# Optimization experiments

Measured on AMD Instinct MI355X. Metric: run time of the kernel, lower is better.

Reference implementation:

```python
import jax, jax.numpy as jnp
import numpy as np

B, L, D, H, F, NL = 8, 1024, 640, 10, 1280, 6
DH = D // H
WINDOW = 64  # spatial-neighbor band half-width
NEG = -1e9


def layer_norm(x, g, b, eps=1e-5):
    m = jnp.mean(x, axis=-1, keepdims=True)
    v = jnp.mean((x - m) ** 2, axis=-1, keepdims=True)
    return (x - m) * jax.lax.rsqrt(v + eps) * g + b


def setup_inputs() -> dict:
    key = jax.random.key(0)
    ks = jax.random.split(key, 20)
    s = 0.02
    x = jax.random.normal(ks[0], (B, L, D), jnp.float32)
    y = jax.random.normal(ks[1], (B, L, D), jnp.float32)
    idx = jnp.arange(L)
    band = jnp.abs(idx[:, None] - idx[None, :]) > WINDOW  # True = disallowed
    x_attn_mask = jnp.broadcast_to(band, (B, L, L))
    y_attn_mask = jnp.broadcast_to(band, (B, L, L))
    x_pad_mask = jnp.zeros((B, L), bool)
    y_pad_mask = jnp.zeros((B, L), bool)
    # stacked per-layer encoder params (torch Linear convention: out = x @ W.T + b)
    params = dict(
        Wqkv=jax.random.normal(ks[2], (NL, 3 * D, D), jnp.float32) * s,
        bqkv=jnp.zeros((NL, 3 * D), jnp.float32),
        Wo=jax.random.normal(ks[3], (NL, D, D), jnp.float32) * s,
        bo=jnp.zeros((NL, D), jnp.float32),
        ln1_g=jnp.ones((NL, D), jnp.float32),
        ln1_b=jnp.zeros((NL, D), jnp.float32),
        W1=jax.random.normal(ks[4], (NL, F, D), jnp.float32) * s,
        b1=jnp.zeros((NL, F), jnp.float32),
        W2=jax.random.normal(ks[5], (NL, D, F), jnp.float32) * s,
        b2=jnp.zeros((NL, D), jnp.float32),
        ln2_g=jnp.ones((NL, D), jnp.float32),
        ln2_b=jnp.zeros((NL, D), jnp.float32),
        lne_g=jnp.ones((D,), jnp.float32),
        lne_b=jnp.zeros((D,), jnp.float32),
        We=jax.random.normal(ks[6], (D, D), jnp.float32) * s,
        be=jnp.zeros((D,), jnp.float32),
    )
    return dict(x=x, x_pad_mask=x_pad_mask, x_attn_mask=x_attn_mask,
                y=y, y_pad_mask=y_pad_mask, y_attn_mask=y_attn_mask, **params)


def _encoder(h, mask_bias, Wqkv, bqkv, Wo, bo, ln1_g, ln1_b, W1, b1, W2, b2, ln2_g, ln2_b):
    scale = 1.0 / np.sqrt(DH)

    def step(h, p):
        (wqkv, bq, wo, bo_, g1, be1, w1, bb1, w2, bb2, g2, be2) = p
        qkv = jnp.einsum('bld,ed->ble', h, wqkv) + bq
        q, k, v = jnp.split(qkv, 3, axis=-1)
        q = q.reshape(B, L, H, DH)
        k = k.reshape(B, L, H, DH)
        v = v.reshape(B, L, H, DH)
        scores = jnp.einsum('blhd,bmhd->bhlm', q, k) * scale + mask_bias  # (B,H,L,L)
        attn = jax.nn.softmax(scores, axis=-1)
        o = jnp.einsum('bhlm,bmhd->blhd', attn, v).reshape(B, L, D)
        o = jnp.einsum('bld,ed->ble', o, wo) + bo_
        h = layer_norm(h + o, g1, be1)  # post-LN (torch default norm_first=False)
        ff = jax.nn.relu(jnp.einsum('bld,fd->blf', h, w1) + bb1)
        ff = jnp.einsum('blf,df->bld', ff, w2) + bb2
        h = layer_norm(h + ff, g2, be2)
        return h, None

    ps = (Wqkv, bqkv, Wo, bo, ln1_g, ln1_b, W1, b1, W2, b2, ln2_g, ln2_b)
    h, _ = jax.lax.scan(step, h, ps)
    return h


def _embed_pool(x, pad_mask, attn_mask, P):
    # bool mask semantics (torch): True = not allowed to attend
    blocked = attn_mask | pad_mask[:, None, :]            # (B,L,L)
    mask_bias = jnp.where(blocked, NEG, 0.0)[:, None]      # (B,1,L,L), shared by heads
    h = _encoder(x, mask_bias, P['Wqkv'], P['bqkv'], P['Wo'], P['bo'],
                 P['ln1_g'], P['ln1_b'], P['W1'], P['b1'], P['W2'], P['b2'],
                 P['ln2_g'], P['ln2_b'])
    pooled = h.sum(axis=1)                                 # (B,D)
    e = layer_norm(pooled, P['lne_g'], P['lne_b'])
    return jax.nn.relu(e @ P['We'].T + P['be'])


def reference(x, x_pad_mask, x_attn_mask, y, y_pad_mask, y_attn_mask,
              Wqkv, bqkv, Wo, bo, ln1_g, ln1_b, W1, b1, W2, b2, ln2_g, ln2_b,
              lne_g, lne_b, We, be):
    P = dict(Wqkv=Wqkv, bqkv=bqkv, Wo=Wo, bo=bo, ln1_g=ln1_g, ln1_b=ln1_b,
             W1=W1, b1=b1, W2=W2, b2=b2, ln2_g=ln2_g, ln2_b=ln2_b,
             lne_g=lne_g, lne_b=lne_b, We=We, be=be)
    ex = _embed_pool(x, x_pad_mask, x_attn_mask, P)
    ey = _embed_pool(y, y_pad_mask, y_attn_mask, P)
    eps = 1e-8
    nx = jnp.maximum(jnp.linalg.norm(ex, axis=-1), eps)
    ny = jnp.maximum(jnp.linalg.norm(ey, axis=-1), eps)
    return jnp.sum(ex * ey, axis=-1) / (nx * ny)  # (B,)
```

## Files before the change

kernel.cpp:

```cpp
#include <hip/hip_runtime.h>


#define LSEQ   1024
#define DMODEL 640
#define NHEAD  10
#define DHEAD  64
#define NLAYER 6
#define BDIM   8
#define FDIM   1280
#define MROWS  (BDIM * LSEQ)

typedef __attribute__((ext_vector_type(8))) _Float16 half8;
typedef __attribute__((ext_vector_type(4))) float    floatx4;

__device__ __forceinline__ void async_copy16(const void* g, void* l) {
  __builtin_amdgcn_global_load_lds(
      (const __attribute__((address_space(1))) void*)g,
      (__attribute__((address_space(3))) void*)l, 16, 0, 0);
}

template <bool RELU, bool RESADD, bool SPLITK>
__global__ __launch_bounds__(256) void gemm_bt(const _Float16* __restrict__ A,
                                               const _Float16* __restrict__ Bw,
                                               const float* __restrict__ bias,
                                               const _Float16* __restrict__ res,
                                               _Float16* __restrict__ Cout,
                                               int M, int N, int K, int ld) {
  __shared__ _Float16 As[2][128 * 32];
  __shared__ _Float16 Bs[2][128 * 32];
  const int m0 = blockIdx.x * 128, n0 = blockIdx.y * 128;
  const int kz = SPLITK ? blockIdx.z : 0;
  const int tid = threadIdx.x;
  const int w = tid >> 6, lane = tid & 63;
  const int quad = lane >> 4, l16 = lane & 15;
  const int wm = w >> 1, wn = w & 1;

  floatx4 acc[4][4];
#pragma unroll
  for (int i = 0; i < 4; i++)
#pragma unroll
    for (int j = 0; j < 4; j++) acc[i][j] = (floatx4){0.f, 0.f, 0.f, 0.f};

  const int arow = w * 16 + (lane >> 2);
  const int kswz = ((lane & 3) ^ ((lane >> 3) & 3)) * 8;
  const _Float16* ag = A + (size_t)(m0 + arow) * ld + kz * K + kswz;
  const _Float16* bg = Bw + (size_t)(n0 + arow) * ld + kz * K + kswz;
  const size_t krows = (size_t)64 * ld;
  const int lofs0 = (w * 16) * 32;
  const int lofs1 = (64 + w * 16) * 32;

  const int fro = l16 * 32 + ((quad ^ ((l16 >> 1) & 3)) * 8);

  const int nIter = K >> 5;
  async_copy16(ag, &As[0][lofs0]);
  async_copy16(ag + krows, &As[0][lofs1]);
  async_copy16(bg, &Bs[0][lofs0]);
  async_copy16(bg + krows, &Bs[0][lofs1]);
  ag += 32; bg += 32;

  for (int i = 0; i < nIter; i++) {
    __syncthreads();
    if (i + 1 < nIter) {
      const int nb = (i + 1) & 1;
      async_copy16(ag, &As[nb][lofs0]);
      async_copy16(ag + krows, &As[nb][lofs1]);
      async_copy16(bg, &Bs[nb][lofs0]);
      async_copy16(bg + krows, &Bs[nb][lofs1]);
      ag += 32; bg += 32;
    }
    const _Float16* as = As[i & 1];
    const _Float16* bs = Bs[i & 1];
    half8 af[4], bf[4];
#pragma unroll
    for (int mt = 0; mt < 4; mt++)
      af[mt] = *(const half8*)&as[(wm * 64 + mt * 16) * 32 + fro];
#pragma unroll
    for (int nt = 0; nt < 4; nt++)
      bf[nt] = *(const half8*)&bs[(wn * 64 + nt * 16) * 32 + fro];
#pragma unroll
    for (int mt = 0; mt < 4; mt++)
#pragma unroll
      for (int nt = 0; nt < 4; nt++)
        acc[mt][nt] = __builtin_amdgcn_mfma_f32_16x16x32_f16(af[mt], bf[nt], acc[mt][nt], 0, 0, 0);
  }

  const bool lead = (!SPLITK) || (kz == 0);
  _Float16* outp = Cout + (SPLITK ? (size_t)kz * ((size_t)M * N) : 0);
  float bv[4];
#pragma unroll
  for (int nt = 0; nt < 4; nt++)
    bv[nt] = lead ? bias[n0 + wn * 64 + nt * 16 + l16] : 0.f;
#pragma unroll
  for (int mt = 0; mt < 4; mt++) {
#pragma unroll
    for (int reg = 0; reg < 4; reg++) {
      const int row = m0 + wm * 64 + mt * 16 + quad * 4 + reg;
#pragma unroll
      for (int nt = 0; nt < 4; nt++) {
        const int col = n0 + wn * 64 + nt * 16 + l16;
        float v = acc[mt][nt][reg] + bv[nt];
        if (RESADD) { if (lead) v += (float)res[(size_t)row * N + col]; }
        if (RELU) v = fmaxf(v, 0.f);
        outp[(size_t)row * N + col] = (_Float16)v;
      }
    }
  }
}

__global__ __launch_bounds__(256) void attn_kernel(const _Float16* __restrict__ qkv,
                                                   _Float16* __restrict__ o) {
  __shared__ _Float16 Qs[64 * 72];
  __shared__ _Float16 KP[192 * 72];
  __shared__ _Float16 Vt[64 * 200];
  const int qb = blockIdx.x, h = blockIdx.y, b = blockIdx.z;
  const int q0 = qb * 64;
  const int kc0 = (q0 - 64 > 0) ? q0 - 64 : 0;
  const int kend = (q0 + 128 < LSEQ) ? q0 + 128 : LSEQ;
  const int cnt = kend - kc0;
  const int tid = threadIdx.x;

  for (int c = tid; c < 512; c += 256) {
    const int row = c >> 3, ch = c & 7;
    *(uint4*)&Qs[row * 72 + ch * 8] =
        *(const uint4*)(qkv + (size_t)(b * LSEQ + q0 + row) * (3 * DMODEL) + h * DHEAD + ch * 8);
  }
  for (int c = tid; c < 1536; c += 256) {
    const int row = c >> 3, ch = c & 7;
    uint4 v = {0u, 0u, 0u, 0u};
    if (row < cnt)
      v = *(const uint4*)(qkv + (size_t)(b * LSEQ + kc0 + row) * (3 * DMODEL) + DMODEL + h * DHEAD + ch * 8);
    *(uint4*)&KP[row * 72 + ch * 8] = v;
  }
  for (int c = tid; c < 1536; c += 256) {
    const int row = c >> 3, ch = c & 7;
    uint4 v = {0u, 0u, 0u, 0u};
    if (row < cnt)
      v = *(const uint4*)(qkv + (size_t)(b * LSEQ + kc0 + row) * (3 * DMODEL) + 2 * DMODEL + h * DHEAD + ch * 8);
    _Float16 tmp[8];
    *(uint4*)tmp = v;
#pragma unroll
    for (int jj = 0; jj < 8; jj++) Vt[(ch * 8 + jj) * 200 + row] = tmp[jj];
  }
  __syncthreads();

  const int w = tid >> 6, lane = tid & 63, quad = lane >> 4, l16 = lane & 15;

  floatx4 sacc[12];
#pragma unroll
  for (int i = 0; i < 12; i++) sacc[i] = (floatx4){0.f, 0.f, 0.f, 0.f};
#pragma unroll
  for (int ks = 0; ks < 2; ks++) {
    const half8 qf = *(const half8*)&Qs[(w * 16 + l16) * 72 + ks * 32 + quad * 8];
#pragma unroll
    for (int nt = 0; nt < 12; nt++) {
      const half8 kf = *(const half8*)&KP[(nt * 16 + l16) * 72 + ks * 32 + quad * 8];
      sacc[nt] = __builtin_amdgcn_mfma_f32_16x16x32_f16(qf, kf, sacc[nt], 0, 0, 0);
    }
  }
  __syncthreads();

#pragma unroll
  for (int r = 0; r < 4; r++) {
    const int qi = q0 + w * 16 + quad * 4 + r;
    float sv[12];
    float m = -1e30f;
#pragma unroll
    for (int nt = 0; nt < 12; nt++) {
      const int key = kc0 + nt * 16 + l16;
      const bool ok = (key >= qi - 64) && (key <= qi + 64) && (key < LSEQ);
      const float s = ok ? sacc[nt][r] * 0.125f : -1e30f;
      sv[nt] = s;
      m = fmaxf(m, s);
    }
#pragma unroll
    for (int d = 1; d < 16; d <<= 1) m = fmaxf(m, __shfl_xor(m, d));
    float sum = 0.f;
#pragma unroll
    for (int nt = 0; nt < 12; nt++) {
      const float p = __expf(sv[nt] - m);
      sv[nt] = p;
      sum += p;
    }
#pragma unroll
    for (int d = 1; d < 16; d <<= 1) sum += __shfl_xor(sum, d);
    const float inv = 1.f / sum;
    _Float16* Pr = &KP[(w * 16 + quad * 4 + r) * 200];
#pragma unroll
    for (int nt = 0; nt < 12; nt++) Pr[nt * 16 + l16] = (_Float16)(sv[nt] * inv);
  }
  __syncthreads();

  floatx4 oacc[4];
#pragma unroll
  for (int i = 0; i < 4; i++) oacc[i] = (floatx4){0.f, 0.f, 0.f, 0.f};
#pragma unroll
  for (int ks = 0; ks < 6; ks++) {
    const half8 pf = *(const half8*)&KP[(w * 16 + l16) * 200 + ks * 32 + quad * 8];
#pragma unroll
    for (int nt = 0; nt < 4; nt++) {
      const half8 vf = *(const half8*)&Vt[(nt * 16 + l16) * 200 + ks * 32 + quad * 8];
      oacc[nt] = __builtin_amdgcn_mfma_f32_16x16x32_f16(pf, vf, oacc[nt], 0, 0, 0);
    }
  }
#pragma unroll
  for (int nt = 0; nt < 4; nt++)
#pragma unroll
    for (int reg = 0; reg < 4; reg++) {
      const int row = q0 + w * 16 + quad * 4 + reg;
      const int col = h * DHEAD + nt * 16 + l16;
      o[(size_t)(b * LSEQ + row) * DMODEL + col] = (_Float16)oacc[nt][reg];
    }
}

__global__ __launch_bounds__(256) void ln_res2_kernel(const _Float16* __restrict__ s0,
                                                      const _Float16* __restrict__ s1,
                                                      const float* __restrict__ g,
                                                      const float* __restrict__ bta,
                                                      _Float16* __restrict__ hh) {
  const int row = blockIdx.x * 4 + (threadIdx.x >> 6);
  const int lane = threadIdx.x & 63;
  const _Float16* p0 = s0 + (size_t)row * DMODEL;
  const _Float16* p1 = s1 + (size_t)row * DMODEL;
  float v[10], s = 0.f, ss = 0.f;
#pragma unroll
  for (int i = 0; i < 10; i++) {
    const float x = (float)p0[lane + 64 * i] + (float)p1[lane + 64 * i];
    v[i] = x; s += x; ss += x * x;
  }
#pragma unroll
  for (int d = 1; d < 64; d <<= 1) { s += __shfl_xor(s, d); ss += __shfl_xor(ss, d); }
  const float mean = s * (1.f / DMODEL);
  const float var = ss * (1.f / DMODEL) - mean * mean;
  const float rstd = rsqrtf(var + 1e-5f);
#pragma unroll
  for (int i = 0; i < 10; i++) {
    const int d = lane + 64 * i;
    hh[(size_t)row * DMODEL + d] = (_Float16)((v[i] - mean) * rstd * g[d] + bta[d]);
  }
}

__global__ void cvt_kernel(const float* __restrict__ s, _Float16* __restrict__ d, int n) {
  int i = blockIdx.x * blockDim.x + threadIdx.x;
  const int stride = gridDim.x * blockDim.x;
  for (; i < n; i += stride) d[i] = (_Float16)s[i];
}

__global__ void zero_kernel(float* __restrict__ p, int n) {
  const int i = blockIdx.x * blockDim.x + threadIdx.x;
  if (i < n) p[i] = 0.f;
}

__global__ void pool_kernel(const _Float16* __restrict__ h, float* __restrict__ pooled) {
  const int b = blockIdx.x, chunk = blockIdx.y;
  for (int d = threadIdx.x; d < DMODEL; d += 256) {
    float s = 0.f;
    const _Float16* p = h + ((size_t)b * LSEQ + chunk * 32) * DMODEL + d;
#pragma unroll 4
    for (int l = 0; l < 32; l++) s += (float)p[(size_t)l * DMODEL];
    atomicAdd(&pooled[b * DMODEL + d], s);
  }
}

__global__ void lnvec_kernel(const float* __restrict__ pooled, const float* __restrict__ g,
                             const float* __restrict__ bta, float* __restrict__ eln) {
  const int b = blockIdx.x, lane = threadIdx.x;
  float v[10], s = 0.f, ss = 0.f;
#pragma unroll
  for (int i = 0; i < 10; i++) {
    const float x = pooled[b * DMODEL + lane + 64 * i];
    v[i] = x; s += x; ss += x * x;
  }
#pragma unroll
  for (int d = 1; d < 64; d <<= 1) { s += __shfl_xor(s, d); ss += __shfl_xor(ss, d); }
  const float mean = s * (1.f / DMODEL);
  const float var = ss * (1.f / DMODEL) - mean * mean;
  const float rstd = rsqrtf(var + 1e-5f);
#pragma unroll
  for (int i = 0; i < 10; i++) {
    const int d = lane + 64 * i;
    eln[b * DMODEL + d] = (v[i] - mean) * rstd * g[d] + bta[d];
  }
}

__global__ __launch_bounds__(256) void embed_kernel(const float* __restrict__ eln,
                                                    const float* __restrict__ We,
                                                    const float* __restrict__ be,
                                                    float* __restrict__ e) {
  const int gw = (blockIdx.x << 2) + (threadIdx.x >> 6);
  const int lane = threadIdx.x & 63;
  const int b = gw / DMODEL, n = gw % DMODEL;
  const float* wr = We + (size_t)n * DMODEL;
  const float* er = eln + (size_t)b * DMODEL;
  float s = 0.f;
#pragma unroll
  for (int i = 0; i < 10; i++) s += wr[lane + 64 * i] * er[lane + 64 * i];
#pragma unroll
  for (int d = 1; d < 64; d <<= 1) s += __shfl_xor(s, d);
  if (lane == 0) e[(size_t)b * DMODEL + n] = fmaxf(s + be[n], 0.f);
}

__global__ void cosine_kernel(const float* __restrict__ ex, const float* __restrict__ ey,
                              float* __restrict__ out) {
  const int b = blockIdx.x, lane = threadIdx.x;
  float sxy = 0.f, sxx = 0.f, syy = 0.f;
#pragma unroll
  for (int i = 0; i < 10; i++) {
    const float x = ex[b * DMODEL + lane + 64 * i];
    const float y = ey[b * DMODEL + lane + 64 * i];
    sxy += x * y; sxx += x * x; syy += y * y;
  }
#pragma unroll
  for (int d = 1; d < 64; d <<= 1) {
    sxy += __shfl_xor(sxy, d); sxx += __shfl_xor(sxx, d); syy += __shfl_xor(syy, d);
  }
  if (lane == 0) {
    const float nx = fmaxf(sqrtf(sxx), 1e-8f);
    const float ny = fmaxf(sqrtf(syy), 1e-8f);
    out[b] = sxy / (nx * ny);
  }
}


extern "C" void kernel_launch(void* const* d_in, const int* in_sizes, int n_in,
                              void* d_out, int out_size, void* d_ws, size_t ws_size,
                              hipStream_t stream) {
  (void)in_sizes; (void)n_in; (void)out_size;
  const float* x    = (const float*)d_in[0];
  const float* y    = (const float*)d_in[3];
  const float* Wqkv = (const float*)d_in[6];
  const float* bqkv = (const float*)d_in[7];
  const float* Wo   = (const float*)d_in[8];
  const float* bo   = (const float*)d_in[9];
  const float* ln1g = (const float*)d_in[10];
  const float* ln1b = (const float*)d_in[11];
  const float* W1   = (const float*)d_in[12];
  const float* b1   = (const float*)d_in[13];
  const float* W2   = (const float*)d_in[14];
  const float* b2   = (const float*)d_in[15];
  const float* ln2g = (const float*)d_in[16];
  const float* ln2b = (const float*)d_in[17];
  const float* lneg = (const float*)d_in[18];
  const float* lneb = (const float*)d_in[19];
  const float* We   = (const float*)d_in[20];
  const float* be   = (const float*)d_in[21];

  auto algn = [](size_t b) { return (b + 255) & ~(size_t)255; };
  const size_t wbytes = algn((size_t)NLAYER * 3 * DMODEL * DMODEL * 2) +
                        algn((size_t)NLAYER * DMODEL * DMODEL * 2) +
                        2 * algn((size_t)NLAYER * FDIM * DMODEL * 2);
  auto actbytes = [&](size_t R) {
    return algn(R * DMODEL * 2) + algn(R * 3 * DMODEL * 2) + algn(R * FDIM * 2) +
           4 * algn((size_t)BDIM * DMODEL * 4);
  };
  const int NS = (wbytes + actbytes((size_t)2 * MROWS) <= ws_size) ? 2 : 1;
  const size_t R = (size_t)NS * MROWS;

  char* ws = (char*)d_ws;
  size_t off = 0;
  auto alloc = [&](size_t bytes) -> char* {
    char* p = ws + off;
    off += algn(bytes);
    return p;
  };
  _Float16* Wqkv_h = (_Float16*)alloc((size_t)NLAYER * 3 * DMODEL * DMODEL * 2);
  _Float16* Wo_h   = (_Float16*)alloc((size_t)NLAYER * DMODEL * DMODEL * 2);
  _Float16* W1_h   = (_Float16*)alloc((size_t)NLAYER * FDIM * DMODEL * 2);
  _Float16* W2_h   = (_Float16*)alloc((size_t)NLAYER * DMODEL * FDIM * 2);
  _Float16* h_h    = (_Float16*)alloc(R * DMODEL * 2);
  _Float16* qkv_h  = (_Float16*)alloc(R * 3 * DMODEL * 2);
  _Float16* ff_h   = (_Float16*)alloc(R * FDIM * 2);
  float*    pooled = (float*)   alloc((size_t)BDIM * DMODEL * 4);
  float*    elnb   = (float*)   alloc((size_t)BDIM * DMODEL * 4);
  float*    exb    = (float*)   alloc((size_t)BDIM * DMODEL * 4);
  float*    eyb    = (float*)   alloc((size_t)BDIM * DMODEL * 4);
  if (off > ws_size) return;
  _Float16* tmp2 = qkv_h;
  _Float16* o_h  = ff_h;

  cvt_kernel<<<2048, 256, 0, stream>>>(Wqkv, Wqkv_h, NLAYER * 3 * DMODEL * DMODEL);
  cvt_kernel<<<2048, 256, 0, stream>>>(Wo,   Wo_h,   NLAYER * DMODEL * DMODEL);
  cvt_kernel<<<2048, 256, 0, stream>>>(W1,   W1_h,   NLAYER * FDIM * DMODEL);
  cvt_kernel<<<2048, 256, 0, stream>>>(W2,   W2_h,   NLAYER * DMODEL * FDIM);

  const float* seq_in[2] = {x, y};
  float* eouts[2] = {exb, eyb};
  const int Mr = (int)R;
  const size_t halfo = (size_t)Mr * DMODEL;

  for (int s0 = 0; s0 < 2; s0 += NS) {
    for (int s = 0; s < NS; s++)
      cvt_kernel<<<2048, 256, 0, stream>>>(
          seq_in[s0 + s], h_h + (size_t)s * MROWS * DMODEL, MROWS * DMODEL);
    for (int l = 0; l < NLAYER; l++) {
      gemm_bt<false, false, false><<<dim3(Mr / 128, 15), 256, 0, stream>>>(
          h_h, Wqkv_h + (size_t)l * 3 * DMODEL * DMODEL, bqkv + l * 3 * DMODEL,
          nullptr, qkv_h, Mr, 3 * DMODEL, DMODEL, DMODEL);
      attn_kernel<<<dim3(LSEQ / 64, NHEAD, Mr / LSEQ), 256, 0, stream>>>(qkv_h, o_h);
      gemm_bt<false, true, true><<<dim3(Mr / 128, 5, 2), 256, 0, stream>>>(
          o_h, Wo_h + (size_t)l * DMODEL * DMODEL, bo + l * DMODEL,
          h_h, tmp2, Mr, DMODEL, DMODEL / 2, DMODEL);
      ln_res2_kernel<<<Mr / 4, 256, 0, stream>>>(
          tmp2, tmp2 + halfo, ln1g + l * DMODEL, ln1b + l * DMODEL, h_h);
      gemm_bt<true, false, false><<<dim3(Mr / 128, 10), 256, 0, stream>>>(
          h_h, W1_h + (size_t)l * FDIM * DMODEL, b1 + l * FDIM,
          nullptr, ff_h, Mr, FDIM, DMODEL, DMODEL);
      gemm_bt<false, true, true><<<dim3(Mr / 128, 5, 2), 256, 0, stream>>>(
          ff_h, W2_h + (size_t)l * DMODEL * FDIM, b2 + l * DMODEL,
          h_h, tmp2, Mr, DMODEL, FDIM / 2, FDIM);
      ln_res2_kernel<<<Mr / 4, 256, 0, stream>>>(
          tmp2, tmp2 + halfo, ln2g + l * DMODEL, ln2b + l * DMODEL, h_h);
    }
    for (int s = 0; s < NS; s++) {
      const _Float16* hseq = h_h + (size_t)s * MROWS * DMODEL;
      zero_kernel<<<(BDIM * DMODEL + 255) / 256, 256, 0, stream>>>(pooled, BDIM * DMODEL);
      pool_kernel<<<dim3(BDIM, 32), 256, 0, stream>>>(hseq, pooled);
      lnvec_kernel<<<BDIM, 64, 0, stream>>>(pooled, lneg, lneb, elnb);
      embed_kernel<<<BDIM * DMODEL / 4, 256, 0, stream>>>(elnb, We, be, eouts[s0 + s]);
    }
  }
  cosine_kernel<<<BDIM, 64, 0, stream>>>(exb, eyb, (float*)d_out);
}
```

Baseline: 1.848 ms.

## Replace async global-to-LDS copies with register-staged prefetch pipeline in GEMM

Drops the direct global_load_lds async copies in the GEMM mainloop. Tiles are now loaded into registers two K-steps ahead and written to the alternate LDS buffer after each MFMA block, with the loop unrolled by two. The aim is to hide global latency behind compute with a deeper prefetch. The cost is higher register pressure and extra LDS store instructions, and the write-after-read ordering between buffers now depends on the barrier placement.

```diff
diff --git a/kernel.cpp b/kernel.cpp
--- a/kernel.cpp
+++ b/kernel.cpp
@@ -12,12 +12,6 @@
 
 typedef __attribute__((ext_vector_type(8))) _Float16 half8;
 typedef __attribute__((ext_vector_type(4))) float    floatx4;
-
-__device__ __forceinline__ void async_copy16(const void* g, void* l) {
-  __builtin_amdgcn_global_load_lds(
-      (const __attribute__((address_space(1))) void*)g,
-      (__attribute__((address_space(3))) void*)l, 16, 0, 0);
-}
 
 template <bool RELU, bool RESADD, bool SPLITK>
 __global__ __launch_bounds__(256) void gemm_bt(const _Float16* __restrict__ A,
@@ -41,47 +35,82 @@
 #pragma unroll
     for (int j = 0; j < 4; j++) acc[i][j] = (floatx4){0.f, 0.f, 0.f, 0.f};
 
-  const int arow = w * 16 + (lane >> 2);
   const int kswz = ((lane & 3) ^ ((lane >> 3) & 3)) * 8;
-  const _Float16* ag = A + (size_t)(m0 + arow) * ld + kz * K + kswz;
-  const _Float16* bg = Bw + (size_t)(n0 + arow) * ld + kz * K + kswz;
+  const _Float16* ag = A + (size_t)(m0 + w * 16 + (lane >> 2)) * ld + kz * K + kswz;
+  const _Float16* bg = Bw + (size_t)(n0 + w * 16 + (lane >> 2)) * ld + kz * K + kswz;
   const size_t krows = (size_t)64 * ld;
-  const int lofs0 = (w * 16) * 32;
-  const int lofs1 = (64 + w * 16) * 32;
+  const int wofs0 = (w * 16 + (lane >> 2)) * 32 + (lane & 3) * 8;
+  const int wofs1 = wofs0 + 64 * 32;
 
   const int fro = l16 * 32 + ((quad ^ ((l16 >> 1) & 3)) * 8);
 
   const int nIter = K >> 5;
-  async_copy16(ag, &As[0][lofs0]);
-  async_copy16(ag + krows, &As[0][lofs1]);
-  async_copy16(bg, &Bs[0][lofs0]);
-  async_copy16(bg + krows, &Bs[0][lofs1]);
+  uint4 a00, a01, b00, b01;
+  uint4 a10, a11, b10, b11;
+  a00 = *(const uint4*)ag; a01 = *(const uint4*)(ag + krows);
+  b00 = *(const uint4*)bg; b01 = *(const uint4*)(bg + krows);
   ag += 32; bg += 32;
-
-  for (int i = 0; i < nIter; i++) {
-    __syncthreads();
+  if (nIter > 1) {
+    a10 = *(const uint4*)ag; a11 = *(const uint4*)(ag + krows);
+    b10 = *(const uint4*)bg; b11 = *(const uint4*)(bg + krows);
+    ag += 32; bg += 32;
+  }
+  *(uint4*)&As[0][wofs0] = a00; *(uint4*)&As[0][wofs1] = a01;
+  *(uint4*)&Bs[0][wofs0] = b00; *(uint4*)&Bs[0][wofs1] = b01;
+
+  for (int i = 0; i < nIter; i += 2) {
+    {
+      __syncthreads();
+      if (i + 2 < nIter) {
+        a00 = *(const uint4*)ag; a01 = *(const uint4*)(ag + krows);
+        b00 = *(const uint4*)bg; b01 = *(const uint4*)(bg + krows);
+        ag += 32; bg += 32;
+      }
+      const _Float16* as = As[0];
+      const _Float16* bs = Bs[0];
+      half8 af[4], bf[4];
+#pragma unroll
+      for (int mt = 0; mt < 4; mt++)
+        af[mt] = *(const half8*)&as[(wm * 64 + mt * 16) * 32 + fro];
+#pragma unroll
+      for (int nt = 0; nt < 4; nt++)
+        bf[nt] = *(const half8*)&bs[(wn * 64 + nt * 16) * 32 + fro];
+#pragma unroll
+      for (int mt = 0; mt < 4; mt++)
+#pragma unroll
+        for (int nt = 0; nt < 4; nt++)
+          acc[mt][nt] = __builtin_amdgcn_mfma_f32_16x16x32_f16(af[mt], bf[nt], acc[mt][nt], 0, 0, 0);
+      if (i + 1 < nIter) {
+        *(uint4*)&As[1][wofs0] = a10; *(uint4*)&As[1][wofs1] = a11;
+        *(uint4*)&Bs[1][wofs0] = b10; *(uint4*)&Bs[1][wofs1] = b11;
+      }
+    }
     if (i + 1 < nIter) {
-      const int nb = (i + 1) & 1;
-      async_copy16(ag, &As[nb][lofs0]);
-      async_copy16(ag + krows, &As[nb][lofs1]);
-      async_copy16(bg, &Bs[nb][lofs0]);
-      async_copy16(bg + krows, &Bs[nb][lofs1]);
-      ag += 32; bg += 32;
-    }
-    const _Float16* as = As[i & 1];
-    const _Float16* bs = Bs[i & 1];
-    half8 af[4], bf[4];
-#pragma unroll
-    for (int mt = 0; mt < 4; mt++)
-      af[mt] = *(const half8*)&as[(wm * 64 + mt * 16) * 32 + fro];
-#pragma unroll
-    for (int nt = 0; nt < 4; nt++)
-      bf[nt] = *(const half8*)&bs[(wn * 64 + nt * 16) * 32 + fro];
-#pragma unroll
-    for (int mt = 0; mt < 4; mt++)
+      __syncthreads();
+      if (i + 3 < nIter) {
+        a10 = *(const uint4*)ag; a11 = *(const uint4*)(ag + krows);
+        b10 = *(const uint4*)bg; b11 = *(const uint4*)(bg + krows);
+        ag += 32; bg += 32;
+      }
+      const _Float16* as = As[1];
+      const _Float16* bs = Bs[1];
+      half8 af[4], bf[4];
+#pragma unroll
+      for (int mt = 0; mt < 4; mt++)
+        af[mt] = *(const half8*)&as[(wm * 64 + mt * 16) * 32 + fro];
 #pragma unroll
       for (int nt = 0; nt < 4; nt++)
-        acc[mt][nt] = __builtin_amdgcn_mfma_f32_16x16x32_f16(af[mt], bf[nt], acc[mt][nt], 0, 0, 0);
+        bf[nt] = *(const half8*)&bs[(wn * 64 + nt * 16) * 32 + fro];
+#pragma unroll
+      for (int mt = 0; mt < 4; mt++)
+#pragma unroll
+        for (int nt = 0; nt < 4; nt++)
+          acc[mt][nt] = __builtin_amdgcn_mfma_f32_16x16x32_f16(af[mt], bf[nt], acc[mt][nt], 0, 0, 0);
+      if (i + 2 < nIter) {
+        *(uint4*)&As[0][wofs0] = a00; *(uint4*)&As[0][wofs1] = a01;
+        *(uint4*)&Bs[0][wofs0] = b00; *(uint4*)&Bs[0][wofs1] = b01;
+      }
+    }
   }
 
   const bool lead = (!SPLITK) || (kz == 0);
```

Result: slower. 2.029 ms (+9.7%).
